# Optimization experiments

Hardware: AMD Instinct MI355X
Metric: run time of the kernel (lower is better)

## Reference

```python
import jax, jax.numpy as jnp
import numpy as np

K = 31          # local attention window (odd)
PAD = (K - 1) // 2
G = 8           # heads / groups
MC = 48         # model_complexity (attention out_features)
OF = 88         # output_features
BN_EPS = 1e-5


def conv2d(x, w, b):
    # x: [B,C,H,W], w: [O,I,3,3], 'SAME' == padding=1 for stride-1 3x3
    y = jax.lax.conv_general_dilated(x, w, (1, 1), 'SAME',
                                     dimension_numbers=('NCHW', 'OIHW', 'NCHW'))
    return y + b[None, :, None, None]


def bn(x, g, b, m, v):
    # inference-mode BatchNorm2d over channel dim of NCHW
    return (x - m[None, :, None, None]) * (g[None, :, None, None] /
           jnp.sqrt(v[None, :, None, None] + BN_EPS)) + b[None, :, None, None]


def maxpool_w2(x):
    # MaxPool2d((1,2)): pool width (freq) by 2
    return jax.lax.reduce_window(x, -jnp.inf, jax.lax.max,
                                 (1, 1, 1, 2), (1, 1, 1, 2), 'VALID')


def setup_inputs() -> dict:
    key = jax.random.key(0)
    ks = jax.random.split(key, 24)
    B, T, F = 8, 2560, 229
    C1, C2 = OF // 16, OF // 8          # 5, 11
    freq_feats = C2 * (F // 2 // 2)      # 11 * 57 = 627
    s = lambda k, shp, sc=0.05: jax.random.normal(k, shp, dtype=jnp.float32) * sc
    inp = {
        'spec':   jax.random.normal(ks[0], (B, T, F), dtype=jnp.float32),
        'c1_w': s(ks[1], (C1, 1, 3, 3)),  'c1_b': s(ks[2], (C1,)),
        'bn1_g': jnp.ones((C1,)), 'bn1_b': jnp.zeros((C1,)),
        'bn1_m': jnp.zeros((C1,)), 'bn1_v': jnp.ones((C1,)),
        'c2_w': s(ks[3], (C1, C1, 3, 3)), 'c2_b': s(ks[4], (C1,)),
        'bn2_g': jnp.ones((C1,)), 'bn2_b': jnp.zeros((C1,)),
        'bn2_m': jnp.zeros((C1,)), 'bn2_v': jnp.ones((C1,)),
        'c3_w': s(ks[5], (C2, C1, 3, 3)), 'c3_b': s(ks[6], (C2,)),
        'bn3_g': jnp.ones((C2,)), 'bn3_b': jnp.zeros((C2,)),
        'bn3_m': jnp.zeros((C2,)), 'bn3_v': jnp.ones((C2,)),
        'fc_w': s(ks[7], (OF, freq_feats)), 'fc_b': s(ks[8], (OF,)),
        'wq': s(ks[9], (MC, OF)), 'wk': s(ks[10], (MC, OF)), 'wv': s(ks[11], (MC, OF)),
        'rel': jax.random.normal(ks[12], (1, MC, K), dtype=jnp.float32),
        'ln_g': jnp.ones((MC,)), 'ln_b': jnp.zeros((MC,)),
        'lin_w': s(ks[13], (OF, MC)), 'lin_b': s(ks[14], (OF,)),
    }
    return inp


def reference(spec, c1_w, c1_b, bn1_g, bn1_b, bn1_m, bn1_v,
              c2_w, c2_b, bn2_g, bn2_b, bn2_m, bn2_v,
              c3_w, c3_b, bn3_g, bn3_b, bn3_m, bn3_v,
              fc_w, fc_b, wq, wk, wv, rel, ln_g, ln_b, lin_w, lin_b):
    B, T, F = spec.shape
    # ---- ConvStack (eval mode: BN uses running stats, dropout = identity) ----
    x = spec[:, None]                                  # [B,1,T,F]
    x = jax.nn.relu(bn(conv2d(x, c1_w, c1_b), bn1_g, bn1_b, bn1_m, bn1_v))
    x = jax.nn.relu(bn(conv2d(x, c2_w, c2_b), bn2_g, bn2_b, bn2_m, bn2_v))
    x = maxpool_w2(x)                                  # F -> F//2
    x = jax.nn.relu(bn(conv2d(x, c3_w, c3_b), bn3_g, bn3_b, bn3_m, bn3_v))
    x = maxpool_w2(x)                                  # F//2 -> F//4
    x = jnp.transpose(x, (0, 2, 1, 3)).reshape(B, T, -1)  # [B,T,C2*(F//4)]
    x = x @ fc_w.T + fc_b                              # [B,T,OF]

    # ---- MutliHeadAttention1D: local windowed attention via unfold ----
    q = x @ wq.T                                       # [B,T,MC]
    xp = jnp.pad(x, ((0, 0), (PAD, PAD), (0, 0)))
    k = xp @ wk.T                                      # [B,T+K-1,MC]
    v = xp @ wv.T
    idx = jnp.arange(T)[:, None] + jnp.arange(K)[None, :]   # [T,K]
    kw = jnp.transpose(k[:, idx], (0, 1, 3, 2)) + rel        # [B,T,MC,K]
    vw = jnp.transpose(v[:, idx], (0, 1, 3, 2))              # [B,T,MC,K]
    Dh = MC // G
    kw = kw.reshape(B, T, G, Dh, K)
    vw = vw.reshape(B, T, G, Dh, K)
    qh = q.reshape(B, T, G, Dh, 1)
    energy = (qh * kw).sum(-2, keepdims=True)          # [B,T,G,1,K]
    attn = jax.nn.softmax(energy, axis=-1)
    out = (attn * vw).sum(-1).reshape(B, T, MC)        # [B,T,MC]
    a = attn.squeeze(3)                                # [B,T,G,K]

    # ---- LayerNorm + Linear + sigmoid ----
    mu = out.mean(-1, keepdims=True)
    var = jnp.mean((out - mu) ** 2, axis=-1, keepdims=True)
    h = (out - mu) / jnp.sqrt(var + 1e-5) * ln_g + ln_b
    frame_pred = jax.nn.sigmoid(h @ lin_w.T + lin_b)   # [B,T,OF]
    return frame_pred, a
```

## Files before the change

kernel.cpp:

```cpp
#include <hip/hip_runtime.h>
#include <hip/hip_bf16.h>
#include <math.h>

#define B_    8
#define T_    2560
#define F_    229
#define C1_   5
#define C2_   11
#define W1_   114
#define W2_   57
#define KP_   640
#define OF_   88
#define MC_   48
#define G_    8
#define DH_   6
#define K_    31
#define PAD_  15
#define BN_EPS 1e-5f
#define LN_EPS 1e-5f
#define TS_   8

typedef __attribute__((ext_vector_type(8))) short short8;
typedef __attribute__((ext_vector_type(4))) float f32x4;

static inline int cdiv(int a, int b) { return (a + b - 1) / b; }

__device__ inline float bflo(unsigned u) { return __uint_as_float(u << 16); }
__device__ inline float bfhi(unsigned u) { return __uint_as_float(u & 0xffff0000u); }

__global__ __launch_bounds__(640, 8) void conv123_kernel(
        const float* __restrict__ spec,
        const float* __restrict__ c1w, const float* __restrict__ c1b,
        const float* __restrict__ g1, const float* __restrict__ b1,
        const float* __restrict__ m1, const float* __restrict__ v1,
        const float* __restrict__ c2w, const float* __restrict__ c2b,
        const float* __restrict__ g2, const float* __restrict__ b2,
        const float* __restrict__ m2, const float* __restrict__ v2,
        const float* __restrict__ c3w, const float* __restrict__ c3b,
        const float* __restrict__ g3, const float* __restrict__ b3,
        const float* __restrict__ m3, const float* __restrict__ v3,
        __hip_bfloat16* __restrict__ x3out) {
    __shared__ ushort x1t[12 * 5 * 232];
    __shared__ float specx2[14 * 232];
    __shared__ float w1s[45], w2s[225], w3s[495];
    __shared__ float scl1[5], shf1[5], scl2[5], shf2[5], scl3[11], shf3[11];
    int t0 = blockIdx.x * TS_;
    int b = blockIdx.y;
    int tid = threadIdx.x;

    if (tid < 45) w1s[tid] = c1w[tid];
    for (int i = tid; i < 225; i += 640) w2s[i] = c2w[i];
    for (int i = tid; i < 495; i += 640) w3s[i] = c3w[i];
    if (tid < 5) {
        float s = g1[tid] * rsqrtf(v1[tid] + BN_EPS);
        scl1[tid] = s;
        shf1[tid] = (c1b[tid] - m1[tid]) * s + b1[tid];
    }
    if (tid >= 64 && tid < 69) {
        int c = tid - 64;
        float s = g2[c] * rsqrtf(v2[c] + BN_EPS);
        scl2[c] = s;
        shf2[c] = (c2b[c] - m2[c]) * s + b2[c];
    }
    if (tid >= 128 && tid < 139) {
        int c = tid - 128;
        float s = g3[c] * rsqrtf(v3[c] + BN_EPS);
        scl3[c] = s;
        shf3[c] = (c3b[c] - m3[c]) * s + b3[c];
    }
    {
        const float* sb = spec + (size_t)b * T_ * F_;
        for (int i = tid; i < 14 * 232; i += 640) {
            int col = i % 232;
            int rr = i / 232;
            int t = t0 - 3 + rr;
            int f = col - 1;
            float v = 0.f;
            if (t >= 0 && t < T_ && f >= 0 && f < F_) v = sb[(size_t)t * F_ + f];
            specx2[i] = v;
        }
    }
    __syncthreads();

    for (int i = tid; i < 12 * 229; i += 640) {
        int f = i % 229;
        int rr = i / 229;
        int t = t0 - 2 + rr;
        float y[5];
        if (t >= 0 && t < T_) {
            float tp[9];
#pragma unroll
            for (int dt = 0; dt < 3; ++dt) {
                const float* row = &specx2[(rr + dt) * 232 + f];
                tp[dt * 3 + 0] = row[0];
                tp[dt * 3 + 1] = row[1];
                tp[dt * 3 + 2] = row[2];
            }
#pragma unroll
            for (int co = 0; co < 5; ++co) {
                float acc = 0.f;
#pragma unroll
                for (int k = 0; k < 9; ++k) acc = fmaf(tp[k], w1s[co * 9 + k], acc);
                y[co] = fmaxf(fmaf(acc, scl1[co], shf1[co]), 0.f);
            }
        } else {
#pragma unroll
            for (int co = 0; co < 5; ++co) y[co] = 0.f;
        }
#pragma unroll
        for (int co = 0; co < 5; ++co) {
            __hip_bfloat16 h = __float2bfloat16(y[co]);
            x1t[(rr * 5 + co) * 232 + 1 + f] = *(ushort*)&h;
        }
    }
    for (int i = tid; i < 180; i += 640) {
        int c = i % 3;
        int col = (c == 0) ? 0 : 229 + c;
        int ci = (i / 3) % 5;
        int rr = i / 15;
        x1t[(rr * 5 + ci) * 232 + col] = 0;
    }
    __syncthreads();

    ushort* x2pt = (ushort*)specx2;
    if (tid < 570) {
        int co = tid / 114;
        int j = tid % 114;
        float acc0[10], acc1[10];
#pragma unroll
        for (int r = 0; r < 10; ++r) { acc0[r] = 0.f; acc1[r] = 0.f; }
#pragma unroll
        for (int ci = 0; ci < 5; ++ci) {
            float wr[9];
#pragma unroll
            for (int k = 0; k < 9; ++k) wr[k] = w2s[(co * 5 + ci) * 9 + k];
#pragma unroll
            for (int rr = 0; rr < 12; ++rr) {
                const ushort* p = &x1t[(rr * 5 + ci) * 232 + 2 * j];
                unsigned u0 = *(const unsigned*)p;
                unsigned u1 = *(const unsigned*)(p + 2);
                float v0 = bflo(u0), v1 = bfhi(u0), v2_ = bflo(u1), v3_ = bfhi(u1);
#pragma unroll
                for (int dt = 0; dt < 3; ++dt) {
                    int r = rr - dt;
                    if (r >= 0 && r < 10) {
                        acc0[r] = fmaf(v0, wr[dt * 3],
                                  fmaf(v1, wr[dt * 3 + 1],
                                  fmaf(v2_, wr[dt * 3 + 2], acc0[r])));
                        acc1[r] = fmaf(v1, wr[dt * 3],
                                  fmaf(v2_, wr[dt * 3 + 1],
                                  fmaf(v3_, wr[dt * 3 + 2], acc1[r])));
                    }
                }
            }
        }
        float s = scl2[co], sh = shf2[co];
        float yv[10];
#pragma unroll
        for (int r = 0; r < 10; ++r) {
            int t = t0 - 1 + r;
            float y = fmaxf(fmaxf(acc0[r] * s + sh, 0.f), fmaxf(acc1[r] * s + sh, 0.f));
            yv[r] = (t < 0 || t >= T_) ? 0.f : y;
        }
        __syncthreads();
#pragma unroll
        for (int r = 0; r < 10; ++r) {
            __hip_bfloat16 h = __float2bfloat16(yv[r]);
            x2pt[(r * 5 + co) * 120 + 1 + j] = *(ushort*)&h;
        }
    } else {
        __syncthreads();
        for (int i = tid - 570; i < 300; i += 70) {
            int cc = i % 6;
            int col = (cc == 0) ? 0 : 114 + cc;
            int ci = (i / 6) % 5;
            int r = i / 30;
            x2pt[(r * 5 + ci) * 120 + col] = 0;
        }
    }
    __syncthreads();

    if (tid < 627) {
        int co = tid / 57;
        int j = tid % 57;
        float acc0[8], acc1[8];
#pragma unroll
        for (int r = 0; r < 8; ++r) { acc0[r] = 0.f; acc1[r] = 0.f; }
#pragma unroll
        for (int ci = 0; ci < 5; ++ci) {
            float wr[9];
#pragma unroll
            for (int k = 0; k < 9; ++k) wr[k] = w3s[(co * 5 + ci) * 9 + k];
#pragma unroll
            for (int rr = 0; rr < 10; ++rr) {
                const ushort* p = &x2pt[(rr * 5 + ci) * 120 + 2 * j];
                unsigned u0 = *(const unsigned*)p;
                unsigned u1 = *(const unsigned*)(p + 2);
                float v0 = bflo(u0), v1 = bfhi(u0), v2_ = bflo(u1), v3_ = bfhi(u1);
#pragma unroll
                for (int dt = 0; dt < 3; ++dt) {
                    int r = rr - dt;
                    if (r >= 0 && r < 8) {
                        acc0[r] = fmaf(v0, wr[dt * 3],
                                  fmaf(v1, wr[dt * 3 + 1],
                                  fmaf(v2_, wr[dt * 3 + 2], acc0[r])));
                        acc1[r] = fmaf(v1, wr[dt * 3],
                                  fmaf(v2_, wr[dt * 3 + 1],
                                  fmaf(v3_, wr[dt * 3 + 2], acc1[r])));
                    }
                }
            }
        }
        float s = scl3[co], sh = shf3[co];
#pragma unroll
        for (int r = 0; r < 8; ++r) {
            float y0 = fmaxf(acc0[r] * s + sh, 0.f);
            float y1 = fmaxf(acc1[r] * s + sh, 0.f);
            x3out[(size_t)(b * T_ + t0 + r) * KP_ + co * 57 + j] =
                __float2bfloat16(fmaxf(y0, y1));
        }
    } else if (tid >= 627 && tid < 640) {
        __hip_bfloat16 z = __float2bfloat16(0.f);
#pragma unroll
        for (int r = 0; r < 8; ++r)
            x3out[(size_t)(b * T_ + t0 + r) * KP_ + tid] = z;
    }
}

__global__ __launch_bounds__(256) void wprime_kernel(const float* __restrict__ fc_w,
        const float* __restrict__ fc_b, const float* __restrict__ wq,
        const float* __restrict__ wk, const float* __restrict__ wv,
        __hip_bfloat16* __restrict__ wp, float* __restrict__ bp) {
    int idx = blockIdx.x * 256 + threadIdx.x;
    if (idx < 144 * KP_) {
        int o = idx / KP_;
        int kk = idx % KP_;
        const float* Wrow = (o < 48) ? (wq + o * 88)
                          : (o < 96) ? (wk + (o - 48) * 88) : (wv + (o - 96) * 88);
        float s = 0.f;
        if (kk < 627)
            for (int i = 0; i < 88; ++i) s = fmaf(Wrow[i], fc_w[(size_t)i * 627 + kk], s);
        wp[idx] = __float2bfloat16(s);
    } else if (idx < 144 * KP_ + 144) {
        int o = idx - 144 * KP_;
        const float* Wrow = (o < 48) ? (wq + o * 88)
                          : (o < 96) ? (wk + (o - 48) * 88) : (wv + (o - 96) * 88);
        float s = 0.f;
        for (int i = 0; i < 88; ++i) s = fmaf(Wrow[i], fc_b[i], s);
        bp[o] = s;
    }
}

__global__ __launch_bounds__(256) void fc_qkv_mfma_kernel(
        const __hip_bfloat16* __restrict__ X, const __hip_bfloat16* __restrict__ Wp,
        const float* __restrict__ bp, float* __restrict__ Q) {
    int tid = threadIdx.x;
    int lane = tid & 63;
    int gw = blockIdx.x * 4 + (tid >> 6);
    int mtile = gw / 3;
    int nthird = gw % 3;
    const short* Xs = (const short*)X;
    const short* Ws = (const short*)Wp;
    int klane = (lane >> 4) * 8;
    const short* xrow = Xs + (size_t)(mtile * 16 + (lane & 15)) * KP_ + klane;
    const short* wrow = Ws + (size_t)(nthird * 48 + (lane & 15)) * KP_ + klane;
    f32x4 acc0 = {0.f, 0.f, 0.f, 0.f}, acc1 = acc0, acc2 = acc0;
#pragma unroll 4
    for (int kt = 0; kt < 20; ++kt) {
        short8 a = *(const short8*)(xrow + kt * 32);
        short8 b0 = *(const short8*)(wrow + kt * 32);
        short8 b1 = *(const short8*)(wrow + 16 * KP_ + kt * 32);
        short8 b2 = *(const short8*)(wrow + 32 * KP_ + kt * 32);
        acc0 = __builtin_amdgcn_mfma_f32_16x16x32_bf16(a, b0, acc0, 0, 0, 0);
        acc1 = __builtin_amdgcn_mfma_f32_16x16x32_bf16(a, b1, acc1, 0, 0, 0);
        acc2 = __builtin_amdgcn_mfma_f32_16x16x32_bf16(a, b2, acc2, 0, 0, 0);
    }
    int r0 = mtile * 16 + (lane >> 4) * 4;
    int col = lane & 15;
    f32x4 accs[3] = {acc0, acc1, acc2};
#pragma unroll
    for (int nt = 0; nt < 3; ++nt) {
        int o = nthird * 48 + nt * 16 + col;
        float bias = bp[o];
#pragma unroll
        for (int rg = 0; rg < 4; ++rg)
            Q[(size_t)(r0 + rg) * 144 + o] = accs[nt][rg] + bias;
    }
}

__global__ __launch_bounds__(256) void attn_ln_kernel(const float* __restrict__ Q,
        const float* __restrict__ rel, const float* __restrict__ lng,
        const float* __restrict__ lnb, const float* __restrict__ lw,
        const float* __restrict__ lb, float* __restrict__ fp,
        float* __restrict__ aout) {
    __shared__ float smem[9472];
    __shared__ float mus[32], rss[32];
    float* kvt = smem;
    float* qt = smem + 6200;
    float* relT = smem + 7864;
    int b = blockIdx.y;
    int t0 = blockIdx.x * 32;
    int tid = threadIdx.x;
    for (int i = tid; i < 62 * 48; i += 256) {
        int row = i / 48, c2 = i % 48;
        int t = t0 - 15 + row;
        float2 v = {0.f, 0.f};
        if (t >= 0 && t < T_)
            v = *(const float2*)&Q[((size_t)b * T_ + t) * 144 + 48 + 2 * c2];
        *(float2*)&kvt[row * 100 + 2 * c2] = v;
    }
    for (int i = tid; i < 32 * 24; i += 256) {
        int row = i / 24, c2 = i % 24;
        float2 v = *(const float2*)&Q[((size_t)b * T_ + t0 + row) * 144 + 2 * c2];
        *(float2*)&qt[row * 52 + 2 * c2] = v;
    }
    for (int i = tid; i < 31 * 48; i += 256) {
        int kp = i / 48, j = i % 48;
        relT[i] = rel[j * 31 + kp];
    }
    __syncthreads();
    int g = tid & 7;
    int tl = tid >> 3;
    const float* qp = &qt[tl * 52 + g * 6];
    float2 q01 = *(const float2*)qp;
    float2 q23 = *(const float2*)(qp + 2);
    float2 q45 = *(const float2*)(qp + 4);
    float e[31];
    float emax = -1e30f;
#pragma unroll
    for (int kp = 0; kp < 31; ++kp) {
        const float* kr = &kvt[(tl + kp) * 100 + g * 6];
        const float* rr = &relT[kp * 48 + g * 6];
        float2 k01 = *(const float2*)kr;
        float2 k23 = *(const float2*)(kr + 2);
        float2 k45 = *(const float2*)(kr + 4);
        float2 r01 = *(const float2*)rr;
        float2 r23 = *(const float2*)(rr + 2);
        float2 r45 = *(const float2*)(rr + 4);
        float s = fmaf(q01.x, k01.x + r01.x,
                  fmaf(q01.y, k01.y + r01.y,
                  fmaf(q23.x, k23.x + r23.x,
                  fmaf(q23.y, k23.y + r23.y,
                  fmaf(q45.x, k45.x + r45.x,
                       q45.y * (k45.y + r45.y))))));
        e[kp] = s;
        emax = fmaxf(emax, s);
    }
    float sum = 0.f;
#pragma unroll
    for (int kp = 0; kp < 31; ++kp) { e[kp] = __expf(e[kp] - emax); sum += e[kp]; }
    float inv = 1.f / sum;
    float o0 = 0, o1 = 0, o2 = 0, o3 = 0, o4 = 0, o5 = 0;
#pragma unroll
    for (int kp = 0; kp < 31; ++kp) {
        float a = e[kp] * inv;
        e[kp] = a;
        const float* vr = &kvt[(tl + kp) * 100 + 48 + g * 6];
        float2 v01 = *(const float2*)vr;
        float2 v23 = *(const float2*)(vr + 2);
        float2 v45 = *(const float2*)(vr + 4);
        o0 = fmaf(a, v01.x, o0); o1 = fmaf(a, v01.y, o1);
        o2 = fmaf(a, v23.x, o2); o3 = fmaf(a, v23.y, o3);
        o4 = fmaf(a, v45.x, o4); o5 = fmaf(a, v45.y, o5);
    }
    __syncthreads();
    float* abuf = smem;
    float* xr = smem + 7936;
#pragma unroll
    for (int kp = 0; kp < 31; ++kp) abuf[tid * 31 + kp] = e[kp];
    {
        float* xp = &xr[tl * 48 + g * 6];
        xp[0] = o0; xp[1] = o1; xp[2] = o2; xp[3] = o3; xp[4] = o4; xp[5] = o5;
    }
    __syncthreads();
    size_t base = ((size_t)b * T_ + t0) * 248;
    for (int i = tid; i < 1984; i += 256) {
        float4 v = *(const float4*)&abuf[4 * i];
        *(float4*)&aout[base + 4 * i] = v;
    }
    if (tid < 32) {
        const float* row = &xr[tid * 48];
        float s = 0.f;
        for (int c = 0; c < 48; ++c) s += row[c];
        float mu = s * (1.f / 48.f);
        float v2 = 0.f;
        for (int c = 0; c < 48; ++c) { float d = row[c] - mu; v2 = fmaf(d, d, v2); }
        mus[tid] = mu;
        rss[tid] = rsqrtf(v2 * (1.f / 48.f) + LN_EPS);
    }
    __syncthreads();
    for (int i = tid; i < 1536; i += 256) {
        int r = i / 48, c = i % 48;
        xr[i] = fmaf((xr[i] - mus[r]) * rss[r], lng[c], lnb[c]);
    }
    __syncthreads();
    size_t obase = ((size_t)b * T_ + t0) * 88;
    for (int k = 0; k < 11; ++k) {
        int cid = k * 256 + tid;
        int o = cid % 88, r = cid / 88;
        const float* xp = &xr[r * 48];
        const float* wpp = &lw[o * 48];
        float s = lb[o];
#pragma unroll
        for (int c = 0; c < 48; c += 4) {
            float4 xv = *(const float4*)&xp[c];
            float4 wv = *(const float4*)&wpp[c];
            s = fmaf(xv.x, wv.x, s);
            s = fmaf(xv.y, wv.y, s);
            s = fmaf(xv.z, wv.z, s);
            s = fmaf(xv.w, wv.w, s);
        }
        fp[obase + cid] = 1.f / (1.f + __expf(-s));
    }
}

extern "C" void kernel_launch(void* const* d_in, const int* in_sizes, int n_in,
                              void* d_out, int out_size, void* d_ws, size_t ws_size,
                              hipStream_t stream) {
    const float* spec = (const float*)d_in[0];
    const float* c1_w = (const float*)d_in[1];
    const float* c1_b = (const float*)d_in[2];
    const float* bn1_g = (const float*)d_in[3];
    const float* bn1_b = (const float*)d_in[4];
    const float* bn1_m = (const float*)d_in[5];
    const float* bn1_v = (const float*)d_in[6];
    const float* c2_w = (const float*)d_in[7];
    const float* c2_b = (const float*)d_in[8];
    const float* bn2_g = (const float*)d_in[9];
    const float* bn2_b = (const float*)d_in[10];
    const float* bn2_m = (const float*)d_in[11];
    const float* bn2_v = (const float*)d_in[12];
    const float* c3_w = (const float*)d_in[13];
    const float* c3_b = (const float*)d_in[14];
    const float* bn3_g = (const float*)d_in[15];
    const float* bn3_b = (const float*)d_in[16];
    const float* bn3_m = (const float*)d_in[17];
    const float* bn3_v = (const float*)d_in[18];
    const float* fc_w = (const float*)d_in[19];
    const float* fc_b = (const float*)d_in[20];
    const float* wq = (const float*)d_in[21];
    const float* wk = (const float*)d_in[22];
    const float* wv = (const float*)d_in[23];
    const float* rel = (const float*)d_in[24];
    const float* ln_g = (const float*)d_in[25];
    const float* ln_b = (const float*)d_in[26];
    const float* lin_w = (const float*)d_in[27];
    const float* lin_b = (const float*)d_in[28];

    float* ws = (float*)d_ws;
    __hip_bfloat16* x3bf = (__hip_bfloat16*)ws;
    __hip_bfloat16* wp_bf = (__hip_bfloat16*)(ws + 19000000);
    float* bp = ws + 19100000;
    float* Qb = ws + 23449600;

    float* frame_pred = (float*)d_out;
    float* a_out = frame_pred + (size_t)B_ * T_ * OF_;

    wprime_kernel<<<cdiv(144 * KP_ + 144, 256), 256, 0, stream>>>(fc_w, fc_b, wq, wk, wv,
                                                                  wp_bf, bp);
    conv123_kernel<<<dim3(T_ / TS_, B_), 640, 0, stream>>>(
        spec, c1_w, c1_b, bn1_g, bn1_b, bn1_m, bn1_v,
        c2_w, c2_b, bn2_g, bn2_b, bn2_m, bn2_v,
        c3_w, c3_b, bn3_g, bn3_b, bn3_m, bn3_v, x3bf);
    fc_qkv_mfma_kernel<<<960, 256, 0, stream>>>(x3bf, wp_bf, bp, Qb);
    attn_ln_kernel<<<dim3(T_ / 32, B_), 256, 0, stream>>>(Qb, rel, ln_g, ln_b, lin_w,
                                                          lin_b, frame_pred, a_out);
}
```

Before: 339.0 us.

## Fuse QKV projection GEMM into the local attention kernel

Merges the MFMA QKV projection and the windowed attention/LayerNorm kernels. Each attention block now computes Q, K and V for its 64-row window (32 frames plus halo) directly into shared memory. This removes the global write and read of the intermediate QKV buffer and one kernel launch. In exchange, the halo rows are recomputed (64 rows per 32 outputs, roughly double the GEMM work), shared memory per block grows, and each wave holds 9 accumulator tiles, which raises register pressure.

New measurement: 359.6 us. 1.06x slower.

```diff
diff --git a/kernel.cpp b/kernel.cpp
--- a/kernel.cpp
+++ b/kernel.cpp
@@ -251,77 +251,68 @@
     }
 }
 
-__global__ __launch_bounds__(256) void fc_qkv_mfma_kernel(
+__global__ __launch_bounds__(256) void attn_fused_kernel(
         const __hip_bfloat16* __restrict__ X, const __hip_bfloat16* __restrict__ Wp,
-        const float* __restrict__ bp, float* __restrict__ Q) {
-    int tid = threadIdx.x;
-    int lane = tid & 63;
-    int gw = blockIdx.x * 4 + (tid >> 6);
-    int mtile = gw / 3;
-    int nthird = gw % 3;
-    const short* Xs = (const short*)X;
-    const short* Ws = (const short*)Wp;
-    int klane = (lane >> 4) * 8;
-    const short* xrow = Xs + (size_t)(mtile * 16 + (lane & 15)) * KP_ + klane;
-    const short* wrow = Ws + (size_t)(nthird * 48 + (lane & 15)) * KP_ + klane;
-    f32x4 acc0 = {0.f, 0.f, 0.f, 0.f}, acc1 = acc0, acc2 = acc0;
-#pragma unroll 4
-    for (int kt = 0; kt < 20; ++kt) {
-        short8 a = *(const short8*)(xrow + kt * 32);
-        short8 b0 = *(const short8*)(wrow + kt * 32);
-        short8 b1 = *(const short8*)(wrow + 16 * KP_ + kt * 32);
-        short8 b2 = *(const short8*)(wrow + 32 * KP_ + kt * 32);
-        acc0 = __builtin_amdgcn_mfma_f32_16x16x32_bf16(a, b0, acc0, 0, 0, 0);
-        acc1 = __builtin_amdgcn_mfma_f32_16x16x32_bf16(a, b1, acc1, 0, 0, 0);
-        acc2 = __builtin_amdgcn_mfma_f32_16x16x32_bf16(a, b2, acc2, 0, 0, 0);
-    }
-    int r0 = mtile * 16 + (lane >> 4) * 4;
-    int col = lane & 15;
-    f32x4 accs[3] = {acc0, acc1, acc2};
-#pragma unroll
-    for (int nt = 0; nt < 3; ++nt) {
-        int o = nthird * 48 + nt * 16 + col;
-        float bias = bp[o];
-#pragma unroll
-        for (int rg = 0; rg < 4; ++rg)
-            Q[(size_t)(r0 + rg) * 144 + o] = accs[nt][rg] + bias;
-    }
-}
-
-__global__ __launch_bounds__(256) void attn_ln_kernel(const float* __restrict__ Q,
-        const float* __restrict__ rel, const float* __restrict__ lng,
-        const float* __restrict__ lnb, const float* __restrict__ lw,
-        const float* __restrict__ lb, float* __restrict__ fp,
-        float* __restrict__ aout) {
-    __shared__ float smem[9472];
+        const float* __restrict__ bp, const float* __restrict__ rel,
+        const float* __restrict__ lng, const float* __restrict__ lnb,
+        const float* __restrict__ lw, const float* __restrict__ lb,
+        float* __restrict__ fp, float* __restrict__ aout) {
+    __shared__ float kvq[64 * 148];
+    __shared__ float relT[31 * 48];
+    __shared__ float biasS[144];
     __shared__ float mus[32], rss[32];
-    float* kvt = smem;
-    float* qt = smem + 6200;
-    float* relT = smem + 7864;
     int b = blockIdx.y;
     int t0 = blockIdx.x * 32;
     int tid = threadIdx.x;
-    for (int i = tid; i < 62 * 48; i += 256) {
-        int row = i / 48, c2 = i % 48;
-        int t = t0 - 15 + row;
-        float2 v = {0.f, 0.f};
-        if (t >= 0 && t < T_)
-            v = *(const float2*)&Q[((size_t)b * T_ + t) * 144 + 48 + 2 * c2];
-        *(float2*)&kvt[row * 100 + 2 * c2] = v;
-    }
-    for (int i = tid; i < 32 * 24; i += 256) {
-        int row = i / 24, c2 = i % 24;
-        float2 v = *(const float2*)&Q[((size_t)b * T_ + t0 + row) * 144 + 2 * c2];
-        *(float2*)&qt[row * 52 + 2 * c2] = v;
-    }
+    int lane = tid & 63;
+    int wave = tid >> 6;
+
     for (int i = tid; i < 31 * 48; i += 256) {
         int kp = i / 48, j = i % 48;
         relT[i] = rel[j * 31 + kp];
     }
-    __syncthreads();
+    if (tid < 144) biasS[tid] = bp[tid];
+    __syncthreads();
+
+    {
+        const short* Xs = (const short*)X;
+        const short* Ws = (const short*)Wp;
+        int rowl = wave * 16 + (lane & 15);
+        int tg = t0 - 15 + rowl;
+        int tc = min(max(tg, 0), T_ - 1);
+        const short* xrow = Xs + ((size_t)(b * T_) + tc) * KP_ + (lane >> 4) * 8;
+        const short* wbase = Ws + (size_t)(lane & 15) * KP_ + (lane >> 4) * 8;
+        f32x4 acc[9];
+#pragma unroll
+        for (int nt = 0; nt < 9; ++nt) acc[nt] = (f32x4){0.f, 0.f, 0.f, 0.f};
+        for (int kt = 0; kt < 20; ++kt) {
+            short8 a = *(const short8*)(xrow + kt * 32);
+#pragma unroll
+            for (int nt = 0; nt < 9; ++nt) {
+                short8 bf = *(const short8*)(wbase + (size_t)nt * 16 * KP_ + kt * 32);
+                acc[nt] = __builtin_amdgcn_mfma_f32_16x16x32_bf16(a, bf, acc[nt], 0, 0, 0);
+            }
+        }
+        int rbase = wave * 16 + (lane >> 4) * 4;
+        int col0 = lane & 15;
+#pragma unroll
+        for (int nt = 0; nt < 9; ++nt) {
+            int col = nt * 16 + col0;
+            float bias = biasS[col];
+#pragma unroll
+            for (int rg = 0; rg < 4; ++rg) {
+                int rl = rbase + rg;
+                int t = t0 - 15 + rl;
+                float v = (t >= 0 && t < T_) ? (acc[nt][rg] + bias) : 0.f;
+                kvq[rl * 148 + col] = v;
+            }
+        }
+    }
+    __syncthreads();
+
     int g = tid & 7;
     int tl = tid >> 3;
-    const float* qp = &qt[tl * 52 + g * 6];
+    const float* qp = &kvq[(15 + tl) * 148 + g * 6];
     float2 q01 = *(const float2*)qp;
     float2 q23 = *(const float2*)(qp + 2);
     float2 q45 = *(const float2*)(qp + 4);
@@ -329,7 +320,7 @@
     float emax = -1e30f;
 #pragma unroll
     for (int kp = 0; kp < 31; ++kp) {
-        const float* kr = &kvt[(tl + kp) * 100 + g * 6];
+        const float* kr = &kvq[(tl + kp) * 148 + 48 + g * 6];
         const float* rr = &relT[kp * 48 + g * 6];
         float2 k01 = *(const float2*)kr;
         float2 k23 = *(const float2*)(kr + 2);
@@ -355,7 +346,7 @@
     for (int kp = 0; kp < 31; ++kp) {
         float a = e[kp] * inv;
         e[kp] = a;
-        const float* vr = &kvt[(tl + kp) * 100 + 48 + g * 6];
+        const float* vr = &kvq[(tl + kp) * 148 + 96 + g * 6];
         float2 v01 = *(const float2*)vr;
         float2 v23 = *(const float2*)(vr + 2);
         float2 v45 = *(const float2*)(vr + 4);
@@ -364,8 +355,8 @@
         o4 = fmaf(a, v45.x, o4); o5 = fmaf(a, v45.y, o5);
     }
     __syncthreads();
-    float* abuf = smem;
-    float* xr = smem + 7936;
+    float* abuf = kvq;
+    float* xr = kvq + 7936;
 #pragma unroll
     for (int kp = 0; kp < 31; ++kp) abuf[tid * 31 + kp] = e[kp];
     {
@@ -451,7 +442,6 @@
     __hip_bfloat16* x3bf = (__hip_bfloat16*)ws;
     __hip_bfloat16* wp_bf = (__hip_bfloat16*)(ws + 19000000);
     float* bp = ws + 19100000;
-    float* Qb = ws + 23449600;
 
     float* frame_pred = (float*)d_out;
     float* a_out = frame_pred + (size_t)B_ * T_ * OF_;
@@ -462,7 +452,6 @@
         spec, c1_w, c1_b, bn1_g, bn1_b, bn1_m, bn1_v,
         c2_w, c2_b, bn2_g, bn2_b, bn2_m, bn2_v,
         c3_w, c3_b, bn3_g, bn3_b, bn3_m, bn3_v, x3bf);
-    fc_qkv_mfma_kernel<<<960, 256, 0, stream>>>(x3bf, wp_bf, bp, Qb);
-    attn_ln_kernel<<<dim3(T_ / 32, B_), 256, 0, stream>>>(Qb, rel, ln_g, ln_b, lin_w,
-                                                          lin_b, frame_pred, a_out);
+    attn_fused_kernel<<<dim3(T_ / 32, B_), 256, 0, stream>>>(
+        x3bf, wp_bf, bp, rel, ln_g, ln_b, lin_w, lin_b, frame_pred, a_out);
 }
```
